# Optimization experiments

Measured on AMD Instinct MI355X. Metric: run time of the kernel, lower is better.

The kernel has to match this reference:

```python
import jax, jax.numpy as jnp
import numpy as np

K = 16
D_MODEL = 128

def _gather(pts, idx):
    # pts: [B,N,C], idx: [B,N,K] -> [B,N,K,C]
    return jax.vmap(lambda p, i: p[i])(pts, idx)

def setup_inputs() -> dict:
    key = jax.random.key(0)
    ks = jax.random.split(key, 20)
    s = 0.05
    def w(k_, shape):
        return jax.random.normal(k_, shape, dtype=jnp.float32) * s
    B, N, C = 4, 4096, 3
    TF, D = 128, D_MODEL
    return {
        "xyz": jax.random.normal(ks[0], (B, N, C), dtype=jnp.float32),
        "W0a": w(ks[1], (C, TF)),  "b0a": jnp.zeros((TF,), jnp.float32),
        "W0b": w(ks[2], (TF, TF)), "b0b": jnp.zeros((TF,), jnp.float32),
        "W1":  w(ks[3], (TF, D)),  "b1":  jnp.zeros((D,), jnp.float32),
        "W2":  w(ks[4], (D, TF)),  "b2":  jnp.zeros((TF,), jnp.float32),
        "Wd1": w(ks[5], (C, D)),   "bd1": jnp.zeros((D,), jnp.float32),
        "Wd2": w(ks[6], (D, D)),   "bd2": jnp.zeros((D,), jnp.float32),
        "Wg1": w(ks[7], (D, D)),   "bg1": jnp.zeros((D,), jnp.float32),
        "Wg2": w(ks[8], (D, D)),   "bg2": jnp.zeros((D,), jnp.float32),
        "Wq":  w(ks[9], (D, D)),
        "Wk":  w(ks[10], (D, D)),
        "Wv":  w(ks[11], (D, D)),
    }

def reference(xyz, W0a, b0a, W0b, b0b, W1, b1, W2, b2,
              Wd1, bd1, Wd2, bd2, Wg1, bg1, Wg2, bg2, Wq, Wk, Wv):
    sq = jnp.sum(xyz * xyz, axis=-1)
    dists = sq[:, :, None] - 2.0 * jnp.einsum('bnc,bmc->bnm', xyz, xyz) + sq[:, None, :]
    _, knn_idx = jax.lax.top_k(-dists, K)          # [B,N,K] nearest neighbors

    knn_xyz = _gather(xyz, knn_idx)                # [B,N,K,3]
    features = jax.nn.relu(xyz @ W0a + b0a) @ W0b + b0b   # fc0  [B,N,TF]
    pre = features
    x = features @ W1 + b1                          # fc1  [B,N,D]
    q = x @ Wq                                      # [B,N,D]
    kf = _gather(x @ Wk, knn_idx)                   # [B,N,K,D]
    vf = _gather(x @ Wv, knn_idx)                   # [B,N,K,D]

    delta = xyz[:, :, None, :] - knn_xyz            # [B,N,K,3]
    pos_enc = jax.nn.relu(delta @ Wd1 + bd1) @ Wd2 + bd2   # fc_delta [B,N,K,D]

    h = q[:, :, None, :] - kf + pos_enc
    attn_logits = jax.nn.relu(h @ Wg1 + bg1) @ Wg2 + bg2   # fc_gamma [B,N,K,D]
    attn = jax.nn.softmax(attn_logits / np.sqrt(D_MODEL).astype(np.float32), axis=-2)

    res = jnp.einsum('bmnf,bmnf->bmf', attn, vf + pos_enc)  # [B,N,D]
    res = res @ W2 + b2 + pre                               # [B,N,TF]
    return res, attn
```

## Files before the change

kernel.cpp:

```cpp
#include <hip/hip_runtime.h>
#include <math.h>

#define BB 4
#define NN 4096
#define KNNK 16
#define DD 128
#define BN (BB*NN)

typedef __attribute__((ext_vector_type(8))) short short8;
typedef __attribute__((ext_vector_type(4))) float floatx4;

__device__ __forceinline__ short f2bf(float x) {
  unsigned u = __float_as_uint(x);
  unsigned r = (u + 0x7fffu + ((u >> 16) & 1u)) >> 16;
  return (short)r;
}

__device__ __forceinline__ float bf2f(short h) {
  return __uint_as_float((unsigned)(unsigned short)h << 16);
}

#define LDSFENCE() asm volatile("s_waitcnt lgkmcnt(0)" ::: "memory")

__device__ __forceinline__ void split_from_lds(const float* __restrict__ trans,
                                               int c, int g, short8 ah[4],
                                               short8 al[4]) {
#pragma unroll
  for (int s = 0; s < 4; ++s) {
    const float* p_ = &trans[c * 132 + s * 32 + g * 8];
    float4 u0 = *reinterpret_cast<const float4*>(p_);
    float4 u1 = *reinterpret_cast<const float4*>(p_ + 4);
    float tmp[8] = {u0.x, u0.y, u0.z, u0.w, u1.x, u1.y, u1.z, u1.w};
#pragma unroll
    for (int j = 0; j < 8; ++j) {
      short h_ = f2bf(tmp[j]);
      ah[s][j] = h_;
      al[s][j] = f2bf(tmp[j] - bf2f(h_));
    }
  }
}

__device__ __forceinline__ void split_gemm2(const short* __restrict__ Bh,
                                            int nt0, int lane,
                                            const short8 ah[4],
                                            const short8 al[4], floatx4& acc0,
                                            floatx4& acc1) {
  const short* Bl = Bh + 16384;
#pragma unroll
  for (int ks = 0; ks < 4; ++ks) {
    const size_t o0 = ((size_t)((nt0 + 0) * 4 + ks) * 64 + lane) * 8;
    const size_t o1 = ((size_t)((nt0 + 1) * 4 + ks) * 64 + lane) * 8;
    short8 bh0 = *reinterpret_cast<const short8*>(Bh + o0);
    short8 bl0 = *reinterpret_cast<const short8*>(Bl + o0);
    short8 bh1 = *reinterpret_cast<const short8*>(Bh + o1);
    short8 bl1 = *reinterpret_cast<const short8*>(Bl + o1);
    acc0 = __builtin_amdgcn_mfma_f32_16x16x32_bf16(ah[ks], bh0, acc0, 0, 0, 0);
    acc1 = __builtin_amdgcn_mfma_f32_16x16x32_bf16(ah[ks], bh1, acc1, 0, 0, 0);
    acc0 = __builtin_amdgcn_mfma_f32_16x16x32_bf16(ah[ks], bl0, acc0, 0, 0, 0);
    acc1 = __builtin_amdgcn_mfma_f32_16x16x32_bf16(ah[ks], bl1, acc1, 0, 0, 0);
    acc0 = __builtin_amdgcn_mfma_f32_16x16x32_bf16(al[ks], bh0, acc0, 0, 0, 0);
    acc1 = __builtin_amdgcn_mfma_f32_16x16x32_bf16(al[ks], bh1, acc1, 0, 0, 0);
  }
}

__device__ __forceinline__ void ced(double& a, double& b) {
  double mn = fmin(a, b);
  double mx = fmax(a, b);
  a = mn;
  b = mx;
}

__device__ __forceinline__ void dsort16(double v[16]) {
#define CE(i, j) ced(v[i], v[j]);
  CE(0, 1) CE(2, 3) CE(4, 5) CE(6, 7) CE(8, 9) CE(10, 11) CE(12, 13) CE(14, 15)
  CE(0, 2) CE(1, 3) CE(4, 6) CE(5, 7) CE(8, 10) CE(9, 11) CE(12, 14) CE(13, 15)
  CE(1, 2) CE(5, 6) CE(9, 10) CE(13, 14)
  CE(0, 4) CE(1, 5) CE(2, 6) CE(3, 7) CE(8, 12) CE(9, 13) CE(10, 14) CE(11, 15)
  CE(2, 4) CE(3, 5) CE(10, 12) CE(11, 13)
  CE(1, 2) CE(3, 4) CE(5, 6) CE(9, 10) CE(11, 12) CE(13, 14)
  CE(0, 8) CE(1, 9) CE(2, 10) CE(3, 11) CE(4, 12) CE(5, 13) CE(6, 14) CE(7, 15)
  CE(4, 8) CE(5, 9) CE(6, 10) CE(7, 11)
  CE(2, 4) CE(3, 5) CE(6, 8) CE(7, 9) CE(10, 12) CE(11, 13)
  CE(1, 2) CE(3, 4) CE(5, 6) CE(7, 8) CE(9, 10) CE(11, 12) CE(13, 14)
#undef CE
}

__device__ __forceinline__ void dbitonic16(double m[16]) {
#pragma unroll
  for (int s = 8; s >= 1; s >>= 1) {
#pragma unroll
    for (int i = 0; i < 16; ++i) {
      if ((i & s) == 0) ced(m[i], m[i + s]);
    }
  }
}

__global__ __launch_bounds__(256, 4) void knn_kernel(const float* __restrict__ xyz,
                                                     int* __restrict__ knn) {
  const int wv = threadIdx.x >> 6;
  const int lane = threadIdx.x & 63;
  const int ln = lane & 15;
  const int qg = lane >> 4;
  const int q = blockIdx.x * 16 + wv * 4 + qg;
  const int b = q >> 12;
  const int n = q & 4095;
  const float* xb = xyz + (size_t)b * NN * 3;

  const float qx = xb[n * 3 + 0], qy = xb[n * 3 + 1], qz = xb[n * 3 + 2];
  const float qsq = __fadd_rn(__fadd_rn(__fmul_rn(qx, qx), __fmul_rn(qy, qy)),
                              __fmul_rn(qz, qz));

#define LOADBATCH(batch)                                                       \
  _Pragma("unroll") for (int i = 0; i < 16; ++i) {                             \
    const int c = ((batch) * 16 + i) * 16 + ln;                                \
    float cx = xb[c * 3 + 0], cy = xb[c * 3 + 1], cz = xb[c * 3 + 2];          \
    float csq = __fadd_rn(__fadd_rn(__fmul_rn(cx, cx), __fmul_rn(cy, cy)),     \
                          __fmul_rn(cz, cz));                                  \
    float dot = __fadd_rn(__fadd_rn(__fmul_rn(qx, cx), __fmul_rn(qy, cy)),     \
                          __fmul_rn(qz, cz));                                  \
    float d = __fadd_rn(__fsub_rn(qsq, __fmul_rn(2.0f, dot)), csq);            \
    unsigned u = __float_as_uint(d);                                           \
    u = (u & 0x80000000u) ? ~u : (u | 0x80000000u);                            \
    unsigned long long key =                                                   \
        0x3FF0000000000000ULL | (((unsigned long long)u << 12) | (unsigned)c); \
    v[i] = __longlong_as_double((long long)key);                               \
  }

  double top[16];
  {
    double v[16];
    LOADBATCH(0);
    dsort16(v);
#pragma unroll
    for (int i = 0; i < 16; ++i) top[i] = v[i];
  }
#pragma unroll 1
  for (int batch = 1; batch < 16; ++batch) {
    double v[16];
    LOADBATCH(batch);
    dsort16(v);
    double m[16];
#pragma unroll
    for (int i = 0; i < 16; ++i)
      m[i] = fmin(top[i], v[15 - i]);
    dbitonic16(m);
#pragma unroll
    for (int i = 0; i < 16; ++i) top[i] = m[i];
  }
#undef LOADBATCH

#pragma unroll
  for (int mask = 1; mask <= 8; mask <<= 1) {
    double oth[16];
#pragma unroll
    for (int i = 0; i < 16; ++i) {
      double y = __shfl_xor(top[15 - i], mask);
      oth[i] = fmin(y, top[i]);
    }
    dbitonic16(oth);
#pragma unroll
    for (int i = 0; i < 16; ++i) top[i] = oth[i];
  }

  if (ln == 0) {
    int* outp = knn + (size_t)q * KNNK;
#pragma unroll
    for (int k = 0; k < 16; ++k)
      outp[k] = (int)(__double_as_longlong(top[k]) & 0xFFFLL);
  }
}

__global__ void swz_all_kernel(const float* __restrict__ Wd2,
                               const float* __restrict__ Wg1,
                               const float* __restrict__ Wg2,
                               const float* __restrict__ W0b,
                               const float* __restrict__ W1,
                               const float* __restrict__ Wq,
                               const float* __restrict__ Wk,
                               const float* __restrict__ Wv,
                               const float* __restrict__ W2,
                               short* __restrict__ wsw,
                               short* __restrict__ wsplit) {
  int t = blockIdx.x * 256 + threadIdx.x;
  if (t < 3 * 2048) {
    int stage = t / 2048;
    int rem = t % 2048;
    int nt = rem / 256;
    int ks = (rem % 256) / 64;
    int lane = rem % 64;
    const float* W = (stage == 0) ? Wd2 : (stage == 1) ? Wg1 : Wg2;
    short8 o;
#pragma unroll
    for (int j = 0; j < 8; ++j) {
      int k = ks * 32 + (lane >> 4) * 8 + j;
      int n = nt * 16 + (lane & 15);
      o[j] = f2bf(W[k * 128 + n]);
    }
    *reinterpret_cast<short8*>(wsw + (size_t)t * 8) = o;
  } else {
    int u = t - 3 * 2048;
    if (u >= 6 * 2048) return;
    int mat = u / 2048;
    int rem = u % 2048;
    int nt = rem / 256;
    int ks = (rem % 256) / 64;
    int lane = rem % 64;
    const float* W = (mat == 0) ? W0b : (mat == 1) ? W1 : (mat == 2) ? Wq
                     : (mat == 3) ? Wk : (mat == 4) ? Wv : W2;
    short8 hi, lo;
#pragma unroll
    for (int j = 0; j < 8; ++j) {
      int k = ks * 32 + (lane >> 4) * 8 + j;
      int n = nt * 16 + (lane & 15);
      float w = W[k * 128 + n];
      short h = f2bf(w);
      hi[j] = h;
      lo[j] = f2bf(w - bf2f(h));
    }
    *reinterpret_cast<short8*>(wsplit + ((size_t)(2 * mat) * 2048 + rem) * 8) = hi;
    *reinterpret_cast<short8*>(wsplit + ((size_t)(2 * mat + 1) * 2048 + rem) * 8) = lo;
  }
}

__global__ __launch_bounds__(256, 4) void point_mlp_mfma_kernel(
    const float* __restrict__ xyz, const float* __restrict__ W0a,
    const float* __restrict__ b0a, const float* __restrict__ b0b,
    const float* __restrict__ b1, const short* __restrict__ wsplit,
    float* __restrict__ pre, float* __restrict__ qv, float* __restrict__ kv,
    float* __restrict__ vv) {
  const int wv = threadIdx.x >> 6;
  const int lane = threadIdx.x & 63;
  const int g = lane >> 4;
  const int c = lane & 15;
  const int g0 = blockIdx.x * 16;
  const int nt0 = wv * 2;

  __shared__ __attribute__((aligned(16))) float trans[16 * 132];
  __shared__ float xs[64];
  if (threadIdx.x < 48) {
    int p = threadIdx.x / 3, cc = threadIdx.x % 3;
    xs[p * 4 + cc] = xyz[(size_t)(g0 + p) * 3 + cc];
  }
  __syncthreads();

  short8 ah[4], al[4];
  {
    const float x0 = xs[c * 4 + 0], x1 = xs[c * 4 + 1], x2 = xs[c * 4 + 2];
#pragma unroll
    for (int s = 0; s < 4; ++s) {
#pragma unroll
      for (int j = 0; j < 8; ++j) {
        const int k = s * 32 + g * 8 + j;
        float v = fmaf(x2, W0a[256 + k],
                       fmaf(x1, W0a[128 + k], fmaf(x0, W0a[k], b0a[k])));
        v = fmaxf(v, 0.f);
        const short h = f2bf(v);
        ah[s][j] = h;
        al[s][j] = f2bf(v - bf2f(h));
      }
    }
  }

  floatx4 acc0, acc1;
  const floatx4 zf = (floatx4){0.f, 0.f, 0.f, 0.f};

  acc0 = zf; acc1 = zf;
  split_gemm2(wsplit + 0 * 32768, nt0, lane, ah, al, acc0, acc1);
  {
    const float bb0 = b0b[nt0 * 16 + c];
    const float bb1 = b0b[(nt0 + 1) * 16 + c];
#pragma unroll
    for (int r = 0; r < 4; ++r) {
      const int row = g * 4 + r;
      float v0 = acc0[r] + bb0;
      float v1 = acc1[r] + bb1;
      pre[(size_t)(g0 + row) * 128 + nt0 * 16 + c] = v0;
      pre[(size_t)(g0 + row) * 128 + (nt0 + 1) * 16 + c] = v1;
      trans[row * 132 + nt0 * 16 + c] = v0;
      trans[row * 132 + (nt0 + 1) * 16 + c] = v1;
    }
  }
  __syncthreads();
  split_from_lds(trans, c, g, ah, al);
  __syncthreads();

  acc0 = zf; acc1 = zf;
  split_gemm2(wsplit + 1 * 32768, nt0, lane, ah, al, acc0, acc1);
  {
    const float bb0 = b1[nt0 * 16 + c];
    const float bb1 = b1[(nt0 + 1) * 16 + c];
#pragma unroll
    for (int r = 0; r < 4; ++r) {
      const int row = g * 4 + r;
      trans[row * 132 + nt0 * 16 + c] = acc0[r] + bb0;
      trans[row * 132 + (nt0 + 1) * 16 + c] = acc1[r] + bb1;
    }
  }
  __syncthreads();
  split_from_lds(trans, c, g, ah, al);
  __syncthreads();

#define GSTORE(dst)                                                            \
  _Pragma("unroll") for (int r = 0; r < 4; ++r) {                              \
    const int row = g0 + g * 4 + r;                                            \
    dst[(size_t)row * 128 + nt0 * 16 + c] = acc0[r];                           \
    dst[(size_t)row * 128 + (nt0 + 1) * 16 + c] = acc1[r];                     \
  }

  acc0 = zf; acc1 = zf;
  split_gemm2(wsplit + 2 * 32768, nt0, lane, ah, al, acc0, acc1);
  GSTORE(qv);

  acc0 = zf; acc1 = zf;
  split_gemm2(wsplit + 3 * 32768, nt0, lane, ah, al, acc0, acc1);
  GSTORE(kv);

  acc0 = zf; acc1 = zf;
  split_gemm2(wsplit + 4 * 32768, nt0, lane, ah, al, acc0, acc1);
  GSTORE(vv);

#undef GSTORE
}

__device__ __forceinline__ void wstage(const short* __restrict__ wsw_stage,
                                       short* __restrict__ wlds, int wv,
                                       int lane) {
#pragma unroll
  for (int i = 0; i < 8; ++i) {
    short8 w_ = *reinterpret_cast<const short8*>(wsw_stage + wv * 4096 +
                                                 i * 512 + lane * 8);
    *reinterpret_cast<short8*>(&wlds[wv * 4096 + i * 512 + lane * 8]) = w_;
  }
}

__global__ __launch_bounds__(256, 3) void attn_mfma_kernel(
    const float* __restrict__ xyz, const int* __restrict__ knn,
    const float* __restrict__ qv, const float* __restrict__ kv,
    const float* __restrict__ vv, const short* __restrict__ wsw,
    const float* __restrict__ Wd1, const float* __restrict__ bd1,
    const float* __restrict__ bd2, const float* __restrict__ bg1,
    const float* __restrict__ bg2, float* __restrict__ res_ws,
    float* __restrict__ out_attn) {
  const int wv = threadIdx.x >> 6;
  const int lane = threadIdx.x & 63;
  const int g = lane >> 4;
  const int c = lane & 15;
  const int bn = blockIdx.x * 4 + wv;
  const int b = bn >> 12;
  const int base_n = b << 12;

  __shared__ __attribute__((aligned(16))) short wlds[16384];
  __shared__ __attribute__((aligned(16))) short conv[4][16 * 136];

  const int* knnp = knn + (size_t)bn * 16;
  const int idxn = knnp[c];
  int idxr[4];
#pragma unroll
  for (int r = 0; r < 4; ++r) idxr[r] = knnp[g * 4 + r];

  float kvf[8][4];
#pragma unroll
  for (int nt = 0; nt < 8; ++nt)
#pragma unroll
    for (int r = 0; r < 4; ++r)
      kvf[nt][r] = kv[((size_t)(base_n + idxr[r])) * 128 + nt * 16 + c];

  const float ddx = xyz[(size_t)bn * 3 + 0] - xyz[((size_t)(base_n + idxn)) * 3 + 0];
  const float ddy = xyz[(size_t)bn * 3 + 1] - xyz[((size_t)(base_n + idxn)) * 3 + 1];
  const float ddz = xyz[(size_t)bn * 3 + 2] - xyz[((size_t)(base_n + idxn)) * 3 + 2];

  short8 af[4];
#pragma unroll
  for (int s = 0; s < 4; ++s) {
#pragma unroll
    for (int j = 0; j < 8; ++j) {
      int d = s * 32 + g * 8 + j;
      float v = fmaf(ddz, Wd1[256 + d],
                     fmaf(ddy, Wd1[128 + d], fmaf(ddx, Wd1[d], bd1[d])));
      af[s][j] = f2bf(fmaxf(v, 0.f));
    }
  }

  float qc[8], bd2v[8];
#pragma unroll
  for (int nt = 0; nt < 8; ++nt) {
    qc[nt] = qv[(size_t)bn * 128 + nt * 16 + c];
    bd2v[nt] = bd2[nt * 16 + c];
  }

  floatx4 acc[8];

#define STAGE_GEMM_LDS()                                                       \
  {                                                                            \
    _Pragma("unroll") for (int ks = 0; ks < 4; ++ks) {                         \
      _Pragma("unroll") for (int h2 = 0; h2 < 2; ++h2) {                       \
        short8 bfr[4];                                                         \
        _Pragma("unroll") for (int i = 0; i < 4; ++i)                          \
          bfr[i] = *reinterpret_cast<const short8*>(                           \
              &wlds[((h2 * 4 + i) * 4 + ks) * 512 + lane * 8]);                \
        _Pragma("unroll") for (int i = 0; i < 4; ++i)                          \
          acc[h2 * 4 + i] = __builtin_amdgcn_mfma_f32_16x16x32_bf16(           \
              af[ks], bfr[i], acc[h2 * 4 + i], 0, 0, 0);                       \
      }                                                                        \
    }                                                                          \
  }

  wstage(wsw, wlds, wv, lane);
  __syncthreads();
#pragma unroll
  for (int nt = 0; nt < 8; ++nt) acc[nt] = (floatx4){0.f, 0.f, 0.f, 0.f};
  STAGE_GEMM_LDS();

  float PE[8][4];
#pragma unroll
  for (int nt = 0; nt < 8; ++nt) {
#pragma unroll
    for (int r = 0; r < 4; ++r) {
      float pe = acc[nt][r] + bd2v[nt];
      PE[nt][r] = pe;
      conv[wv][(g * 4 + r) * 136 + nt * 16 + c] =
          f2bf(qc[nt] - kvf[nt][r] + pe);
    }
  }
  LDSFENCE();
#pragma unroll
  for (int s = 0; s < 4; ++s)
    af[s] = *reinterpret_cast<const short8*>(&conv[wv][c * 136 + s * 32 + g * 8]);

  __syncthreads();
  wstage(wsw + 16384, wlds, wv, lane);
  __syncthreads();
#pragma unroll
  for (int nt = 0; nt < 8; ++nt) acc[nt] = (floatx4){0.f, 0.f, 0.f, 0.f};
  STAGE_GEMM_LDS();
#pragma unroll
  for (int nt = 0; nt < 8; ++nt) {
    const float bg1v = bg1[nt * 16 + c];
#pragma unroll
    for (int r = 0; r < 4; ++r) {
      conv[wv][(g * 4 + r) * 136 + nt * 16 + c] =
          f2bf(fmaxf(acc[nt][r] + bg1v, 0.f));
    }
  }
  LDSFENCE();
#pragma unroll
  for (int s = 0; s < 4; ++s)
    af[s] = *reinterpret_cast<const short8*>(&conv[wv][c * 136 + s * 32 + g * 8]);

  __syncthreads();
  wstage(wsw + 32768, wlds, wv, lane);
  __syncthreads();

  const float inv = 0.0883883476483184f;
  float resv[8];
#pragma unroll
  for (int h = 0; h < 2; ++h) {
    const int ntb = h * 4;
    float vvf[4][4];
#pragma unroll
    for (int i = 0; i < 4; ++i)
#pragma unroll
      for (int r = 0; r < 4; ++r)
        vvf[i][r] =
            vv[((size_t)(base_n + idxr[r])) * 128 + (ntb + i) * 16 + c];

    floatx4 acch[4];
#pragma unroll
    for (int i = 0; i < 4; ++i) acch[i] = (floatx4){0.f, 0.f, 0.f, 0.f};
#pragma unroll
    for (int ks = 0; ks < 4; ++ks) {
      short8 bfr[4];
#pragma unroll
      for (int i = 0; i < 4; ++i)
        bfr[i] = *reinterpret_cast<const short8*>(
            &wlds[((ntb + i) * 4 + ks) * 512 + lane * 8]);
#pragma unroll
      for (int i = 0; i < 4; ++i)
        acch[i] = __builtin_amdgcn_mfma_f32_16x16x32_bf16(af[ks], bfr[i],
                                                          acch[i], 0, 0, 0);
    }

#pragma unroll
    for (int i = 0; i < 4; ++i) {
      const int nt = ntb + i;
      const float bg2v = bg2[nt * 16 + c];
      float l0 = (acch[i][0] + bg2v) * inv;
      float l1 = (acch[i][1] + bg2v) * inv;
      float l2 = (acch[i][2] + bg2v) * inv;
      float l3 = (acch[i][3] + bg2v) * inv;
      float m4 = fmaxf(fmaxf(l0, l1), fmaxf(l2, l3));
      m4 = fmaxf(m4, __shfl_xor(m4, 16));
      m4 = fmaxf(m4, __shfl_xor(m4, 32));
      float e0 = expf(l0 - m4), e1 = expf(l1 - m4);
      float e2 = expf(l2 - m4), e3 = expf(l3 - m4);
      float s4 = e0 + e1 + e2 + e3;
      s4 += __shfl_xor(s4, 16);
      s4 += __shfl_xor(s4, 32);
      float rs = 1.f / s4;
      float a0 = e0 * rs, a1 = e1 * rs, a2 = e2 * rs, a3 = e3 * rs;
      size_t base = ((size_t)bn * 16 + g * 4) * 128 + nt * 16 + c;
      out_attn[base + 0 * 128] = a0;
      out_attn[base + 1 * 128] = a1;
      out_attn[base + 2 * 128] = a2;
      out_attn[base + 3 * 128] = a3;
      float r = 0.f;
      r = fmaf(a0, vvf[i][0] + PE[nt][0], r);
      r = fmaf(a1, vvf[i][1] + PE[nt][1], r);
      r = fmaf(a2, vvf[i][2] + PE[nt][2], r);
      r = fmaf(a3, vvf[i][3] + PE[nt][3], r);
      r += __shfl_xor(r, 16);
      r += __shfl_xor(r, 32);
      resv[nt] = r;
    }
  }
#undef STAGE_GEMM_LDS

  if (g == 0) {
#pragma unroll
    for (int nt = 0; nt < 8; ++nt)
      res_ws[(size_t)bn * 128 + nt * 16 + c] = resv[nt];
  }
}

__global__ __launch_bounds__(256, 4) void epilogue_mfma_kernel(
    const float* __restrict__ res_ws, const short* __restrict__ wsplit,
    const float* __restrict__ b2, const float* __restrict__ pre,
    float* __restrict__ out_res) {
  const int wv = threadIdx.x >> 6;
  const int lane = threadIdx.x & 63;
  const int g = lane >> 4;
  const int c = lane & 15;
  const int g0 = blockIdx.x * 16;
  const int nt0 = wv * 2;

  __shared__ __attribute__((aligned(16))) float trans[16 * 132];

#pragma unroll
  for (int i = 0; i < 2; ++i) {
    int idx4 = threadIdx.x + i * 256;
    int row = idx4 >> 5;
    int col4 = idx4 & 31;
    float4 v = *reinterpret_cast<const float4*>(
        res_ws + (size_t)(g0 + row) * 128 + col4 * 4);
    *reinterpret_cast<float4*>(&trans[row * 132 + col4 * 4]) = v;
  }
  __syncthreads();

  short8 ah[4], al[4];
  split_from_lds(trans, c, g, ah, al);

  float prv0[4], prv1[4];
  const float bb0 = b2[nt0 * 16 + c];
  const float bb1 = b2[(nt0 + 1) * 16 + c];
#pragma unroll
  for (int r = 0; r < 4; ++r) {
    prv0[r] = pre[(size_t)(g0 + g * 4 + r) * 128 + nt0 * 16 + c];
    prv1[r] = pre[(size_t)(g0 + g * 4 + r) * 128 + (nt0 + 1) * 16 + c];
  }

  floatx4 acc0 = (floatx4){0.f, 0.f, 0.f, 0.f};
  floatx4 acc1 = (floatx4){0.f, 0.f, 0.f, 0.f};
  split_gemm2(wsplit + 5 * 32768, nt0, lane, ah, al, acc0, acc1);

#pragma unroll
  for (int r = 0; r < 4; ++r) {
    const int row = g0 + g * 4 + r;
    out_res[(size_t)row * 128 + nt0 * 16 + c] = acc0[r] + bb0 + prv0[r];
    out_res[(size_t)row * 128 + (nt0 + 1) * 16 + c] = acc1[r] + bb1 + prv1[r];
  }
}

extern "C" void kernel_launch(void* const* d_in, const int* in_sizes, int n_in,
                              void* d_out, int out_size, void* d_ws,
                              size_t ws_size, hipStream_t stream) {
  const float* xyz = (const float*)d_in[0];
  const float* W0a = (const float*)d_in[1];
  const float* b0a = (const float*)d_in[2];
  const float* W0b = (const float*)d_in[3];
  const float* b0b = (const float*)d_in[4];
  const float* W1 = (const float*)d_in[5];
  const float* b1 = (const float*)d_in[6];
  const float* W2 = (const float*)d_in[7];
  const float* b2 = (const float*)d_in[8];
  const float* Wd1 = (const float*)d_in[9];
  const float* bd1 = (const float*)d_in[10];
  const float* Wd2 = (const float*)d_in[11];
  const float* bd2 = (const float*)d_in[12];
  const float* Wg1 = (const float*)d_in[13];
  const float* bg1 = (const float*)d_in[14];
  const float* Wg2 = (const float*)d_in[15];
  const float* bg2 = (const float*)d_in[16];
  const float* Wq = (const float*)d_in[17];
  const float* Wk = (const float*)d_in[18];
  const float* Wv = (const float*)d_in[19];

  char* ws = (char*)d_ws;
  int* knn = (int*)ws;
  float* pre = (float*)(ws + (1 << 20));
  float* qv = (float*)(ws + (9 << 20));
  float* kv = (float*)(ws + (17 << 20));
  float* vv = (float*)(ws + (25 << 20));
  float* res_ws = (float*)(ws + (33 << 20));
  short* wsw = (short*)(ws + (41 << 20));
  short* wsplit = (short*)(ws + (41 << 20) + (128 << 10));

  float* out_res = (float*)d_out;
  float* out_attn = out_res + (size_t)BN * DD;

  hipLaunchKernelGGL(swz_all_kernel, dim3(72), dim3(256), 0, stream, Wd2, Wg1,
                     Wg2, W0b, W1, Wq, Wk, Wv, W2, wsw, wsplit);
  hipLaunchKernelGGL(knn_kernel, dim3(1024), dim3(256), 0, stream, xyz, knn);
  hipLaunchKernelGGL(point_mlp_mfma_kernel, dim3(1024), dim3(256), 0, stream,
                     xyz, W0a, b0a, b0b, b1, wsplit, pre, qv, kv, vv);
  hipLaunchKernelGGL(attn_mfma_kernel, dim3(4096), dim3(256), 0, stream, xyz,
                     knn, qv, kv, vv, wsw, Wd1, bd1, bd2, bg1, bg2, res_ws,
                     out_attn);
  hipLaunchKernelGGL(epilogue_mfma_kernel, dim3(1024), dim3(256), 0, stream,
                     res_ws, wsplit, b2, pre, out_res);
}
```

Measured before the change: 345.9 us.

## Merge kNN and point-MLP kernels into one launch and use fast exp

```diff
diff --git a/kernel.cpp b/kernel.cpp
--- a/kernel.cpp
+++ b/kernel.cpp
@@ -95,13 +95,13 @@
   }
 }
 
-__global__ __launch_bounds__(256, 4) void knn_kernel(const float* __restrict__ xyz,
-                                                     int* __restrict__ knn) {
+__device__ void knn_body(int qblk16, const float* __restrict__ xyz,
+                         int* __restrict__ knn) {
   const int wv = threadIdx.x >> 6;
   const int lane = threadIdx.x & 63;
   const int ln = lane & 15;
   const int qg = lane >> 4;
-  const int q = blockIdx.x * 16 + wv * 4 + qg;
+  const int q = qblk16 * 16 + wv * 4 + qg;
   const int b = q >> 12;
   const int n = q & 4095;
   const float* xb = xyz + (size_t)b * NN * 3;
@@ -167,6 +167,124 @@
 #pragma unroll
     for (int k = 0; k < 16; ++k)
       outp[k] = (int)(__double_as_longlong(top[k]) & 0xFFFLL);
+  }
+}
+
+__device__ void mlp_body(int blk, float* __restrict__ trans,
+                         float* __restrict__ xs, const float* __restrict__ xyz,
+                         const float* __restrict__ W0a,
+                         const float* __restrict__ b0a,
+                         const float* __restrict__ b0b,
+                         const float* __restrict__ b1,
+                         const short* __restrict__ wsplit,
+                         float* __restrict__ pre, float* __restrict__ qv,
+                         float* __restrict__ kv, float* __restrict__ vv) {
+  const int wv = threadIdx.x >> 6;
+  const int lane = threadIdx.x & 63;
+  const int g = lane >> 4;
+  const int c = lane & 15;
+  const int g0 = blk * 16;
+  const int nt0 = wv * 2;
+
+  if (threadIdx.x < 48) {
+    int p = threadIdx.x / 3, cc = threadIdx.x % 3;
+    xs[p * 4 + cc] = xyz[(size_t)(g0 + p) * 3 + cc];
+  }
+  __syncthreads();
+
+  short8 ah[4], al[4];
+  {
+    const float x0 = xs[c * 4 + 0], x1 = xs[c * 4 + 1], x2 = xs[c * 4 + 2];
+#pragma unroll
+    for (int s = 0; s < 4; ++s) {
+#pragma unroll
+      for (int j = 0; j < 8; ++j) {
+        const int k = s * 32 + g * 8 + j;
+        float v = fmaf(x2, W0a[256 + k],
+                       fmaf(x1, W0a[128 + k], fmaf(x0, W0a[k], b0a[k])));
+        v = fmaxf(v, 0.f);
+        const short h = f2bf(v);
+        ah[s][j] = h;
+        al[s][j] = f2bf(v - bf2f(h));
+      }
+    }
+  }
+
+  floatx4 acc0, acc1;
+  const floatx4 zf = (floatx4){0.f, 0.f, 0.f, 0.f};
+
+  acc0 = zf; acc1 = zf;
+  split_gemm2(wsplit + 0 * 32768, nt0, lane, ah, al, acc0, acc1);
+  {
+    const float bb0 = b0b[nt0 * 16 + c];
+    const float bb1 = b0b[(nt0 + 1) * 16 + c];
+#pragma unroll
+    for (int r = 0; r < 4; ++r) {
+      const int row = g * 4 + r;
+      float v0 = acc0[r] + bb0;
+      float v1 = acc1[r] + bb1;
+      pre[(size_t)(g0 + row) * 128 + nt0 * 16 + c] = v0;
+      pre[(size_t)(g0 + row) * 128 + (nt0 + 1) * 16 + c] = v1;
+      trans[row * 132 + nt0 * 16 + c] = v0;
+      trans[row * 132 + (nt0 + 1) * 16 + c] = v1;
+    }
+  }
+  __syncthreads();
+  split_from_lds(trans, c, g, ah, al);
+  __syncthreads();
+
+  acc0 = zf; acc1 = zf;
+  split_gemm2(wsplit + 1 * 32768, nt0, lane, ah, al, acc0, acc1);
+  {
+    const float bb0 = b1[nt0 * 16 + c];
+    const float bb1 = b1[(nt0 + 1) * 16 + c];
+#pragma unroll
+    for (int r = 0; r < 4; ++r) {
+      const int row = g * 4 + r;
+      trans[row * 132 + nt0 * 16 + c] = acc0[r] + bb0;
+      trans[row * 132 + (nt0 + 1) * 16 + c] = acc1[r] + bb1;
+    }
+  }
+  __syncthreads();
+  split_from_lds(trans, c, g, ah, al);
+  __syncthreads();
+
+#define GSTORE(dst)                                                            \
+  _Pragma("unroll") for (int r = 0; r < 4; ++r) {                              \
+    const int row = g0 + g * 4 + r;                                            \
+    dst[(size_t)row * 128 + nt0 * 16 + c] = acc0[r];                           \
+    dst[(size_t)row * 128 + (nt0 + 1) * 16 + c] = acc1[r];                     \
+  }
+
+  acc0 = zf; acc1 = zf;
+  split_gemm2(wsplit + 2 * 32768, nt0, lane, ah, al, acc0, acc1);
+  GSTORE(qv);
+
+  acc0 = zf; acc1 = zf;
+  split_gemm2(wsplit + 3 * 32768, nt0, lane, ah, al, acc0, acc1);
+  GSTORE(kv);
+
+  acc0 = zf; acc1 = zf;
+  split_gemm2(wsplit + 4 * 32768, nt0, lane, ah, al, acc0, acc1);
+  GSTORE(vv);
+
+#undef GSTORE
+}
+
+__global__ __launch_bounds__(256, 4) void knn_mlp_kernel(
+    const float* __restrict__ xyz, int* __restrict__ knn,
+    const float* __restrict__ W0a, const float* __restrict__ b0a,
+    const float* __restrict__ b0b, const float* __restrict__ b1,
+    const short* __restrict__ wsplit, float* __restrict__ pre,
+    float* __restrict__ qv, float* __restrict__ kv, float* __restrict__ vv) {
+  __shared__ __attribute__((aligned(16))) float trans[16 * 132];
+  __shared__ float xs[64];
+  const int bid = blockIdx.x;
+  if (bid & 1) {
+    mlp_body(bid >> 1, trans, xs, xyz, W0a, b0a, b0b, b1, wsplit, pre, qv, kv,
+             vv);
+  } else {
+    knn_body(bid >> 1, xyz, knn);
   }
 }
 
@@ -222,106 +340,6 @@
   }
 }
 
-__global__ __launch_bounds__(256, 4) void point_mlp_mfma_kernel(
-    const float* __restrict__ xyz, const float* __restrict__ W0a,
-    const float* __restrict__ b0a, const float* __restrict__ b0b,
-    const float* __restrict__ b1, const short* __restrict__ wsplit,
-    float* __restrict__ pre, float* __restrict__ qv, float* __restrict__ kv,
-    float* __restrict__ vv) {
-  const int wv = threadIdx.x >> 6;
-  const int lane = threadIdx.x & 63;
-  const int g = lane >> 4;
-  const int c = lane & 15;
-  const int g0 = blockIdx.x * 16;
-  const int nt0 = wv * 2;
-
-  __shared__ __attribute__((aligned(16))) float trans[16 * 132];
-  __shared__ float xs[64];
-  if (threadIdx.x < 48) {
-    int p = threadIdx.x / 3, cc = threadIdx.x % 3;
-    xs[p * 4 + cc] = xyz[(size_t)(g0 + p) * 3 + cc];
-  }
-  __syncthreads();
-
-  short8 ah[4], al[4];
-  {
-    const float x0 = xs[c * 4 + 0], x1 = xs[c * 4 + 1], x2 = xs[c * 4 + 2];
-#pragma unroll
-    for (int s = 0; s < 4; ++s) {
-#pragma unroll
-      for (int j = 0; j < 8; ++j) {
-        const int k = s * 32 + g * 8 + j;
-        float v = fmaf(x2, W0a[256 + k],
-                       fmaf(x1, W0a[128 + k], fmaf(x0, W0a[k], b0a[k])));
-        v = fmaxf(v, 0.f);
-        const short h = f2bf(v);
-        ah[s][j] = h;
-        al[s][j] = f2bf(v - bf2f(h));
-      }
-    }
-  }
-
-  floatx4 acc0, acc1;
-  const floatx4 zf = (floatx4){0.f, 0.f, 0.f, 0.f};
-
-  acc0 = zf; acc1 = zf;
-  split_gemm2(wsplit + 0 * 32768, nt0, lane, ah, al, acc0, acc1);
-  {
-    const float bb0 = b0b[nt0 * 16 + c];
-    const float bb1 = b0b[(nt0 + 1) * 16 + c];
-#pragma unroll
-    for (int r = 0; r < 4; ++r) {
-      const int row = g * 4 + r;
-      float v0 = acc0[r] + bb0;
-      float v1 = acc1[r] + bb1;
-      pre[(size_t)(g0 + row) * 128 + nt0 * 16 + c] = v0;
-      pre[(size_t)(g0 + row) * 128 + (nt0 + 1) * 16 + c] = v1;
-      trans[row * 132 + nt0 * 16 + c] = v0;
-      trans[row * 132 + (nt0 + 1) * 16 + c] = v1;
-    }
-  }
-  __syncthreads();
-  split_from_lds(trans, c, g, ah, al);
-  __syncthreads();
-
-  acc0 = zf; acc1 = zf;
-  split_gemm2(wsplit + 1 * 32768, nt0, lane, ah, al, acc0, acc1);
-  {
-    const float bb0 = b1[nt0 * 16 + c];
-    const float bb1 = b1[(nt0 + 1) * 16 + c];
-#pragma unroll
-    for (int r = 0; r < 4; ++r) {
-      const int row = g * 4 + r;
-      trans[row * 132 + nt0 * 16 + c] = acc0[r] + bb0;
-      trans[row * 132 + (nt0 + 1) * 16 + c] = acc1[r] + bb1;
-    }
-  }
-  __syncthreads();
-  split_from_lds(trans, c, g, ah, al);
-  __syncthreads();
-
-#define GSTORE(dst)                                                            \
-  _Pragma("unroll") for (int r = 0; r < 4; ++r) {                              \
-    const int row = g0 + g * 4 + r;                                            \
-    dst[(size_t)row * 128 + nt0 * 16 + c] = acc0[r];                           \
-    dst[(size_t)row * 128 + (nt0 + 1) * 16 + c] = acc1[r];                     \
-  }
-
-  acc0 = zf; acc1 = zf;
-  split_gemm2(wsplit + 2 * 32768, nt0, lane, ah, al, acc0, acc1);
-  GSTORE(qv);
-
-  acc0 = zf; acc1 = zf;
-  split_gemm2(wsplit + 3 * 32768, nt0, lane, ah, al, acc0, acc1);
-  GSTORE(kv);
-
-  acc0 = zf; acc1 = zf;
-  split_gemm2(wsplit + 4 * 32768, nt0, lane, ah, al, acc0, acc1);
-  GSTORE(vv);
-
-#undef GSTORE
-}
-
 __device__ __forceinline__ void wstage(const short* __restrict__ wsw_stage,
                                        short* __restrict__ wlds, int wv,
                                        int lane) {
@@ -491,8 +509,8 @@
       float m4 = fmaxf(fmaxf(l0, l1), fmaxf(l2, l3));
       m4 = fmaxf(m4, __shfl_xor(m4, 16));
       m4 = fmaxf(m4, __shfl_xor(m4, 32));
-      float e0 = expf(l0 - m4), e1 = expf(l1 - m4);
-      float e2 = expf(l2 - m4), e3 = expf(l3 - m4);
+      float e0 = __expf(l0 - m4), e1 = __expf(l1 - m4);
+      float e2 = __expf(l2 - m4), e3 = __expf(l3 - m4);
       float s4 = e0 + e1 + e2 + e3;
       s4 += __shfl_xor(s4, 16);
       s4 += __shfl_xor(s4, 32);
@@ -609,9 +627,8 @@
 
   hipLaunchKernelGGL(swz_all_kernel, dim3(72), dim3(256), 0, stream, Wd2, Wg1,
                      Wg2, W0b, W1, Wq, Wk, Wv, W2, wsw, wsplit);
-  hipLaunchKernelGGL(knn_kernel, dim3(1024), dim3(256), 0, stream, xyz, knn);
-  hipLaunchKernelGGL(point_mlp_mfma_kernel, dim3(1024), dim3(256), 0, stream,
-                     xyz, W0a, b0a, b0b, b1, wsplit, pre, qv, kv, vv);
+  hipLaunchKernelGGL(knn_mlp_kernel, dim3(2048), dim3(256), 0, stream, xyz,
+                     knn, W0a, b0a, b0b, b1, wsplit, pre, qv, kv, vv);
   hipLaunchKernelGGL(attn_mfma_kernel, dim3(4096), dim3(256), 0, stream, xyz,
                      knn, qv, kv, vv, wsw, Wd1, bd1, bd2, bg1, bg2, res_ws,
                      out_attn);
```

After: 439.9 us. +27.2%, slower.
